# Kernel optimization log

Measured on AMD Instinct MI355X. Metric: run time of the kernel, lower is better.

## Reference

```python
import jax, jax.numpy as jnp
import numpy as np
from jax import lax

RATIO = 2.0
ITERATIONS = 1


def setup_inputs() -> dict:
    key = jax.random.key(0)
    k1, k2 = jax.random.split(key)
    N, H, W = 64, 512, 512
    x = jax.random.normal(k1, (N, H, W), dtype=jnp.float32)  # logits
    y = jax.random.randint(k2, (N, H, W), 0, 2, dtype=jnp.int32)  # binary labels
    return {"x": x, "y": y}


def _erode(m):
    # cv2.erode with 3x3 all-ones kernel == 3x3 min-pool; cv2 default border
    # value for erode is +inf, matching reduce_window's init_value padding.
    return lax.reduce_window(m, jnp.inf, lax.min, (1, 3, 3), (1, 1, 1), 'SAME')


def _dilate(m):
    # cv2.dilate == 3x3 max-pool; default border value -inf == init_value pad.
    return lax.reduce_window(m, -jnp.inf, lax.max, (1, 3, 3), (1, 1, 1), 'SAME')


def reference(x, y):
    yf = y.astype(x.dtype)
    # elementwise BCE-with-logits (reduction='none'), numerically stable
    loss = jnp.maximum(x, 0.0) - x * yf + jnp.log1p(jnp.exp(-jnp.abs(x)))
    m = (y > 0).astype(x.dtype)  # [N,H,W] binary mask
    ero, dil = m, m
    for _ in range(ITERATIONS):
        ero = _erode(ero)
        dil = _dilate(dil)
    border = dil - ero  # 1 on border pixels, 0 elsewhere
    w = border * RATIO + (1.0 - border)
    return (loss * w).mean()
```

## Files before the change

### kernel.cpp

```cpp
#include <hip/hip_runtime.h>
#include <math.h>

#define NIMG 64
#define HH 512
#define WW 512
#define NPIX (NIMG * HH * WW)
#define NTHREADS (NPIX / 4)
#define NBLK (NTHREADS / 256)
#define INV_TOTAL (1.0f / 16777216.0f)

__global__ __launch_bounds__(256, 8) void border_loss_main(
    const float* __restrict__ x, const int* __restrict__ y,
    float* __restrict__ part, int atomic_mode)
{
    __shared__ float wsum[4];

    const int tid = threadIdx.x;
    const int idx = blockIdx.x * 256 + tid;
    const int g   = idx & 127;
    const int r   = (idx >> 7) & (HH - 1);
    const int n   = idx >> 16;
    const int rowb = n * (HH * WW) + r * WW;
    const int c0  = g << 2;

    const int offT = (r > 0)      ? -WW : 0;
    const int offB = (r < HH - 1) ?  WW : 0;
    const int cL   = (g == 0)     ? 0        : (c0 - 1);
    const int cR   = (g == 127)   ? (WW - 1) : (c0 + 4);

    const int4 yC = *(const int4*)(y + rowb + c0);
    const int4 yT = *(const int4*)(y + rowb + offT + c0);
    const int4 yB = *(const int4*)(y + rowb + offB + c0);
    const int yCL = y[rowb + cL];
    const int yTL = y[rowb + offT + cL];
    const int yBL = y[rowb + offB + cL];
    const int yCR = y[rowb + cR];
    const int yTR = y[rowb + offT + cR];
    const int yBR = y[rowb + offB + cR];
    const float4 xv = *(const float4*)(x + rowb + c0);

    const int vo0 = yT.x | yC.x | yB.x;
    const int vo1 = yT.y | yC.y | yB.y;
    const int vo2 = yT.z | yC.z | yB.z;
    const int vo3 = yT.w | yC.w | yB.w;
    const int va0 = yT.x & yC.x & yB.x;
    const int va1 = yT.y & yC.y & yB.y;
    const int va2 = yT.z & yC.z & yB.z;
    const int va3 = yT.w & yC.w & yB.w;
    const int voL = yTL | yCL | yBL;
    const int vaL = yTL & yCL & yBL;
    const int voR = yTR | yCR | yBR;
    const int vaR = yTR & yCR & yBR;

    const int ho0 = voL | vo0 | vo1;
    const int ho1 = vo0 | vo1 | vo2;
    const int ho2 = vo1 | vo2 | vo3;
    const int ho3 = vo2 | vo3 | voR;
    const int ha0 = vaL & va0 & va1;
    const int ha1 = va0 & va1 & va2;
    const int ha2 = va1 & va2 & va3;
    const int ha3 = va2 & va3 & vaR;

    float acc;
    {
        const float xf = xv.x;
        const float lg = __logf(1.0f + __expf(-fabsf(xf)));
        const float ls = fmaxf(xf, 0.0f) - (yC.x ? xf : 0.0f) + lg;
        const bool bd = (ho0 != 0) & (ha0 == 0);
        acc = ls * (bd ? 2.0f : 1.0f);
    }
    {
        const float xf = xv.y;
        const float lg = __logf(1.0f + __expf(-fabsf(xf)));
        const float ls = fmaxf(xf, 0.0f) - (yC.y ? xf : 0.0f) + lg;
        const bool bd = (ho1 != 0) & (ha1 == 0);
        acc = fmaf(ls, bd ? 2.0f : 1.0f, acc);
    }
    {
        const float xf = xv.z;
        const float lg = __logf(1.0f + __expf(-fabsf(xf)));
        const float ls = fmaxf(xf, 0.0f) - (yC.z ? xf : 0.0f) + lg;
        const bool bd = (ho2 != 0) & (ha2 == 0);
        acc = fmaf(ls, bd ? 2.0f : 1.0f, acc);
    }
    {
        const float xf = xv.w;
        const float lg = __logf(1.0f + __expf(-fabsf(xf)));
        const float ls = fmaxf(xf, 0.0f) - (yC.w ? xf : 0.0f) + lg;
        const bool bd = (ho3 != 0) & (ha3 == 0);
        acc = fmaf(ls, bd ? 2.0f : 1.0f, acc);
    }

    #pragma unroll
    for (int off = 32; off > 0; off >>= 1)
        acc += __shfl_down(acc, off);
    if ((tid & 63) == 0) wsum[tid >> 6] = acc;
    __syncthreads();
    if (tid == 0) {
        const float t = wsum[0] + wsum[1] + wsum[2] + wsum[3];
        if (atomic_mode) atomicAdd(part, t * INV_TOTAL);
        else             part[blockIdx.x] = t;
    }
}

__global__ __launch_bounds__(256) void border_loss_reduce(
    const float* __restrict__ part, float* __restrict__ out)
{
    __shared__ float wsum[4];
    float t = 0.0f;
    for (int i = threadIdx.x; i < NBLK; i += 256) t += part[i];
    #pragma unroll
    for (int off = 32; off > 0; off >>= 1)
        t += __shfl_down(t, off);
    if ((threadIdx.x & 63) == 0) wsum[threadIdx.x >> 6] = t;
    __syncthreads();
    if (threadIdx.x == 0)
        out[0] = (wsum[0] + wsum[1] + wsum[2] + wsum[3]) * INV_TOTAL;
}

__global__ void border_loss_zero(float* out) { out[0] = 0.0f; }

extern "C" void kernel_launch(void* const* d_in, const int* in_sizes, int n_in,
                              void* d_out, int out_size, void* d_ws, size_t ws_size,
                              hipStream_t stream)
{
    const float* x = (const float*)d_in[0];
    const int*   y = (const int*)d_in[1];
    float* out = (float*)d_out;

    if (ws_size >= (size_t)NBLK * sizeof(float)) {
        float* part = (float*)d_ws;
        border_loss_main<<<NBLK, 256, 0, stream>>>(x, y, part, 0);
        border_loss_reduce<<<1, 256, 0, stream>>>(part, out);
    } else {
        border_loss_zero<<<1, 1, 0, stream>>>(out);
        border_loss_main<<<NBLK, 256, 0, stream>>>(x, y, out, 1);
    }
}
```

Before: 159.6 us.

## Map one wavefront per row with 8 pixels per lane and shuffle halos

Each thread now handles 8 consecutive pixels, so a 64-lane wavefront covers a full 512-wide row. The left and right neighbour column values come from wavefront shuffles instead of six scalar halo loads per thread. The loss math is simplified: the label select is folded into fmax and the border weight is computed as 1 + (or ^ and), which assumes 0/1 labels. The grid is halved, giving more work per thread and fewer redundant loads, at the cost of more registers per thread.

```diff
diff --git a/kernel.cpp b/kernel.cpp
--- a/kernel.cpp
+++ b/kernel.cpp
@@ -4,9 +4,7 @@
 #define NIMG 64
 #define HH 512
 #define WW 512
-#define NPIX (NIMG * HH * WW)
-#define NTHREADS (NPIX / 4)
-#define NBLK (NTHREADS / 256)
+#define NBLK 8192
 #define INV_TOTAL (1.0f / 16777216.0f)
 
 __global__ __launch_bounds__(256, 8) void border_loss_main(
@@ -15,81 +13,68 @@
 {
     __shared__ float wsum[4];
 
-    const int tid = threadIdx.x;
-    const int idx = blockIdx.x * 256 + tid;
-    const int g   = idx & 127;
-    const int r   = (idx >> 7) & (HH - 1);
-    const int n   = idx >> 16;
+    const int tid  = threadIdx.x;
+    const int idx  = blockIdx.x * 256 + tid;
+    const int lane = tid & 63;
+    const int r    = (idx >> 6) & (HH - 1);
+    const int n    = idx >> 15;
     const int rowb = n * (HH * WW) + r * WW;
-    const int c0  = g << 2;
+    const int col  = lane << 3;
 
-    const int offT = (r > 0)      ? -WW : 0;
-    const int offB = (r < HH - 1) ?  WW : 0;
-    const int cL   = (g == 0)     ? 0        : (c0 - 1);
-    const int cR   = (g == 127)   ? (WW - 1) : (c0 + 4);
+    const int pC = rowb + col;
+    const int pT = pC + ((r > 0)      ? -WW : 0);
+    const int pB = pC + ((r < HH - 1) ?  WW : 0);
 
-    const int4 yC = *(const int4*)(y + rowb + c0);
-    const int4 yT = *(const int4*)(y + rowb + offT + c0);
-    const int4 yB = *(const int4*)(y + rowb + offB + c0);
-    const int yCL = y[rowb + cL];
-    const int yTL = y[rowb + offT + cL];
-    const int yBL = y[rowb + offB + cL];
-    const int yCR = y[rowb + cR];
-    const int yTR = y[rowb + offT + cR];
-    const int yBR = y[rowb + offB + cR];
-    const float4 xv = *(const float4*)(x + rowb + c0);
+    const int4   t0 = *(const int4*)(y + pT);
+    const int4   t1 = *(const int4*)(y + pT + 4);
+    const int4   c0 = *(const int4*)(y + pC);
+    const int4   c1 = *(const int4*)(y + pC + 4);
+    const int4   b0 = *(const int4*)(y + pB);
+    const int4   b1 = *(const int4*)(y + pB + 4);
+    const float4 xa = *(const float4*)(x + pC);
+    const float4 xb = *(const float4*)(x + pC + 4);
 
-    const int vo0 = yT.x | yC.x | yB.x;
-    const int vo1 = yT.y | yC.y | yB.y;
-    const int vo2 = yT.z | yC.z | yB.z;
-    const int vo3 = yT.w | yC.w | yB.w;
-    const int va0 = yT.x & yC.x & yB.x;
-    const int va1 = yT.y & yC.y & yB.y;
-    const int va2 = yT.z & yC.z & yB.z;
-    const int va3 = yT.w & yC.w & yB.w;
-    const int voL = yTL | yCL | yBL;
-    const int vaL = yTL & yCL & yBL;
-    const int voR = yTR | yCR | yBR;
-    const int vaR = yTR & yCR & yBR;
+    const int vo0 = t0.x | c0.x | b0.x;  const int va0 = t0.x & c0.x & b0.x;
+    const int vo1 = t0.y | c0.y | b0.y;  const int va1 = t0.y & c0.y & b0.y;
+    const int vo2 = t0.z | c0.z | b0.z;  const int va2 = t0.z & c0.z & b0.z;
+    const int vo3 = t0.w | c0.w | b0.w;  const int va3 = t0.w & c0.w & b0.w;
+    const int vo4 = t1.x | c1.x | b1.x;  const int va4 = t1.x & c1.x & b1.x;
+    const int vo5 = t1.y | c1.y | b1.y;  const int va5 = t1.y & c1.y & b1.y;
+    const int vo6 = t1.z | c1.z | b1.z;  const int va6 = t1.z & c1.z & b1.z;
+    const int vo7 = t1.w | c1.w | b1.w;  const int va7 = t1.w & c1.w & b1.w;
 
-    const int ho0 = voL | vo0 | vo1;
-    const int ho1 = vo0 | vo1 | vo2;
-    const int ho2 = vo1 | vo2 | vo3;
-    const int ho3 = vo2 | vo3 | voR;
-    const int ha0 = vaL & va0 & va1;
-    const int ha1 = va0 & va1 & va2;
-    const int ha2 = va1 & va2 & va3;
-    const int ha3 = va2 & va3 & vaR;
+    const int iL = (lane + 63) & 63, iR = (lane + 1) & 63;
+    const int voLs = __shfl(vo7, iL), vaLs = __shfl(va7, iL);
+    const int voRs = __shfl(vo0, iR), vaRs = __shfl(va0, iR);
+    const int voL = (lane == 0)  ? vo0 : voLs;
+    const int vaL = (lane == 0)  ? va0 : vaLs;
+    const int voR = (lane == 63) ? vo7 : voRs;
+    const int vaR = (lane == 63) ? va7 : vaRs;
 
-    float acc;
-    {
-        const float xf = xv.x;
-        const float lg = __logf(1.0f + __expf(-fabsf(xf)));
-        const float ls = fmaxf(xf, 0.0f) - (yC.x ? xf : 0.0f) + lg;
-        const bool bd = (ho0 != 0) & (ha0 == 0);
-        acc = ls * (bd ? 2.0f : 1.0f);
-    }
-    {
-        const float xf = xv.y;
-        const float lg = __logf(1.0f + __expf(-fabsf(xf)));
-        const float ls = fmaxf(xf, 0.0f) - (yC.y ? xf : 0.0f) + lg;
-        const bool bd = (ho1 != 0) & (ha1 == 0);
-        acc = fmaf(ls, bd ? 2.0f : 1.0f, acc);
-    }
-    {
-        const float xf = xv.z;
-        const float lg = __logf(1.0f + __expf(-fabsf(xf)));
-        const float ls = fmaxf(xf, 0.0f) - (yC.z ? xf : 0.0f) + lg;
-        const bool bd = (ho2 != 0) & (ha2 == 0);
-        acc = fmaf(ls, bd ? 2.0f : 1.0f, acc);
-    }
-    {
-        const float xf = xv.w;
-        const float lg = __logf(1.0f + __expf(-fabsf(xf)));
-        const float ls = fmaxf(xf, 0.0f) - (yC.w ? xf : 0.0f) + lg;
-        const bool bd = (ho3 != 0) & (ha3 == 0);
-        acc = fmaf(ls, bd ? 2.0f : 1.0f, acc);
-    }
+    const int ho0 = voL | vo0 | vo1;  const int ha0 = vaL & va0 & va1;
+    const int ho1 = vo0 | vo1 | vo2;  const int ha1 = va0 & va1 & va2;
+    const int ho2 = vo1 | vo2 | vo3;  const int ha2 = va1 & va2 & va3;
+    const int ho3 = vo2 | vo3 | vo4;  const int ha3 = va2 & va3 & va4;
+    const int ho4 = vo3 | vo4 | vo5;  const int ha4 = va3 & va4 & va5;
+    const int ho5 = vo4 | vo5 | vo6;  const int ha5 = va4 & va5 & va6;
+    const int ho6 = vo5 | vo6 | vo7;  const int ha6 = va5 & va6 & va7;
+    const int ho7 = vo6 | vo7 | voR;  const int ha7 = va6 & va7 & vaR;
+
+    float acc = 0.0f;
+#define PX(xf, m, ho, ha) { \
+        const float ls = fmaxf((m) ? -(xf) : (xf), 0.0f) \
+                       + __logf(1.0f + __expf(-fabsf(xf))); \
+        const float wf = (float)(1 + ((ho) ^ (ha))); \
+        acc = fmaf(ls, wf, acc); }
+    PX(xa.x, c0.x, ho0, ha0)
+    PX(xa.y, c0.y, ho1, ha1)
+    PX(xa.z, c0.z, ho2, ha2)
+    PX(xa.w, c0.w, ho3, ha3)
+    PX(xb.x, c1.x, ho4, ha4)
+    PX(xb.y, c1.y, ho5, ha5)
+    PX(xb.z, c1.z, ho6, ha6)
+    PX(xb.w, c1.w, ho7, ha7)
+#undef PX
 
     #pragma unroll
     for (int off = 32; off > 0; off >>= 1)
```

Result: faster. 148.5 us (-7.0%).
